# Optimization experiments

Measured on AMD Instinct MI355X. Metric: run time of the kernel, lower is better.

## Reference

```python
import jax, jax.numpy as jnp
import numpy as np

SLOPE = 0.2  # leaky_relu_slope for both LVC block and kernel predictor (passed through)
DILATIONS = (1, 3, 9, 27)
HOP = 256
STRIDE = 8
IN_CH = 32
KSZ = 3  # conv_kernel_size


def conv1d(x, w, b, dilation=1, padding=0):
    # x: (B,C,T), w: (O,I,K) torch layout
    y = jax.lax.conv_general_dilated(
        x, w, window_strides=(1,), padding=[(padding, padding)],
        rhs_dilation=(dilation,), dimension_numbers=('NCH', 'OIH', 'NCH'))
    return y + b[None, :, None]


def conv_transpose1d(x, w, b, stride, padding, output_padding=0):
    # w: torch ConvTranspose1d layout (Cin, Cout, K)
    w_ = jnp.flip(w, -1).transpose(1, 0, 2)  # (Cout, Cin, K)
    K = w.shape[2]
    pad = (K - 1 - padding, K - 1 - padding + output_padding)
    y = jax.lax.conv_general_dilated(
        x, w_, window_strides=(1,), padding=[pad],
        lhs_dilation=(stride,), dimension_numbers=('NCH', 'OIH', 'NCH'))
    return y + b[None, :, None]


def lrelu(x, slope=SLOPE):
    return jnp.where(x >= 0, x, slope * x)


def location_variable_convolution(x, kernel, bias, hop):
    # x: (B,C,T), kernel: (B,C,O,k,L), bias: (B,O,L); T == L*hop; dilation==1 path
    B, C, T = x.shape
    _, _, O, k, L = kernel.shape
    pad = (k - 1) // 2
    xp = jnp.pad(x, ((0, 0), (0, 0), (pad, pad)))
    # gather per-segment sliding windows: (L, hop, k) index into time axis
    idx = (jnp.arange(L)[:, None, None] * hop
           + jnp.arange(hop)[None, :, None]
           + jnp.arange(k)[None, None, :])
    xw = xp[:, :, idx]  # (B, C, L, hop, k)
    o = jnp.einsum('bclsk,bcokl->bols', xw, kernel)  # (B, O, L, hop)
    o = o + bias[:, :, :, None]
    return o.reshape(B, O, L * hop)


def kernel_predictor(spec, kp_in_w, kp_in_b, rb_w1, rb_b1, rb_w2, rb_b2,
                     kern_w, kern_b, bias_w, bias_b):
    B, _, L = spec.shape
    h = conv1d(spec, kp_in_w, kp_in_b, padding=2)  # k=5, pad=2
    for i in range(3):  # num_blocks = 3
        r = h
        h = conv1d(h, rb_w1[i], rb_b1[i], padding=1)
        h = lrelu(h)
        h = conv1d(h, rb_w2[i], rb_b2[i], padding=1)
        h = lrelu(h) + r
    kh = conv1d(h, kern_w, kern_b, padding=1)
    bh = conv1d(h, bias_w, bias_b, padding=1)
    n_layers = len(DILATIONS)
    kernels = kh.reshape(B, n_layers, IN_CH, 2 * IN_CH, KSZ, L)
    biases = bh.reshape(B, n_layers, 2 * IN_CH, L)
    return kernels, biases


def reference(hidden_states, spectrogram, convt_w, convt_b, kp_in_w, kp_in_b,
              rb_w1, rb_b1, rb_w2, rb_b2, kern_w, kern_b, bias_w, bias_b,
              lvc_w, lvc_b):
    h = conv_transpose1d(hidden_states, convt_w, convt_b,
                         stride=STRIDE, padding=STRIDE // 2 + STRIDE % 2,
                         output_padding=STRIDE % 2)
    kernels, biases = kernel_predictor(spectrogram, kp_in_w, kp_in_b,
                                       rb_w1, rb_b1, rb_w2, rb_b2,
                                       kern_w, kern_b, bias_w, bias_b)
    for i, d in enumerate(DILATIONS):
        r = h
        h = lrelu(h)
        h = conv1d(h, lvc_w[i], lvc_b[i], dilation=d, padding=d * (KSZ - 1) // 2)
        h = lrelu(h)
        h = location_variable_convolution(h, kernels[:, i], biases[:, i], HOP)
        h = jax.nn.sigmoid(h[:, :IN_CH, :]) * jnp.tanh(h[:, IN_CH:, :]) + r
    return h


def setup_inputs() -> dict:
    key = jax.random.key(0)
    ks = jax.random.split(key, 12)
    B, COND, L, H = 4, 100, 256, 64
    T = L * HOP  # 65536 output samples
    s = jnp.float32(0.02)
    d = {}
    d['hidden_states'] = jax.random.normal(ks[0], (B, IN_CH, T // STRIDE), jnp.float32)
    d['spectrogram'] = jax.random.normal(ks[1], (B, COND, L), jnp.float32)
    d['convt_w'] = jax.random.normal(ks[2], (IN_CH, IN_CH, 2 * STRIDE), jnp.float32) * s
    d['convt_b'] = jnp.zeros((IN_CH,), jnp.float32)
    d['kp_in_w'] = jax.random.normal(ks[3], (H, COND, 5), jnp.float32) * s
    d['kp_in_b'] = jnp.zeros((H,), jnp.float32)
    d['rb_w1'] = jax.random.normal(ks[4], (3, H, H, 3), jnp.float32) * s
    d['rb_b1'] = jnp.zeros((3, H), jnp.float32)
    d['rb_w2'] = jax.random.normal(ks[5], (3, H, H, 3), jnp.float32) * s
    d['rb_b2'] = jnp.zeros((3, H), jnp.float32)
    KC = IN_CH * 2 * IN_CH * KSZ * len(DILATIONS)  # 24576
    d['kern_w'] = jax.random.normal(ks[6], (KC, H, 3), jnp.float32) * s
    d['kern_b'] = jnp.zeros((KC,), jnp.float32)
    BC = 2 * IN_CH * len(DILATIONS)  # 256
    d['bias_w'] = jax.random.normal(ks[7], (BC, H, 3), jnp.float32) * s
    d['bias_b'] = jnp.zeros((BC,), jnp.float32)
    d['lvc_w'] = jax.random.normal(ks[8], (len(DILATIONS), IN_CH, IN_CH, 3), jnp.float32) * s
    d['lvc_b'] = jnp.zeros((len(DILATIONS), IN_CH), jnp.float32)
    return d
```

## Files before the change

### kernel.cpp

```cpp
#include <hip/hip_runtime.h>
#include <math.h>

#define NB 4
#define T 65536
#define TIN 8192
#define LL 256
#define KCL 6144

__device__ __forceinline__ float lrelu_f(float v) { return v >= 0.f ? v : 0.2f * v; }

union Phase1LDS {
    struct { float xs[32][264]; float wm[64][128]; } cvt;
    struct { float hs[64][56]; float xsp[20][56]; float wt[192][68]; } trk;
};

__global__ void __launch_bounds__(512) phase1(
    const float* __restrict__ x, const float* __restrict__ cw,
    const float* __restrict__ cbias, float* __restrict__ hout,
    const float* __restrict__ spec,
    const float* __restrict__ kp_in_w, const float* __restrict__ kp_in_b,
    const float* __restrict__ rb_w1, const float* __restrict__ rb_b1,
    const float* __restrict__ rb_w2, const float* __restrict__ rb_b2,
    float* __restrict__ kp_h) {
    __shared__ Phase1LDS u;
    const int bid = blockIdx.x;
    const int tid = threadIdx.x;
    const int lane = tid & 63, wv = tid >> 6;

    if (bid < 264) {
        const int bx = bid % 33;
        const int rr = bid / 33;
        const int mtp = rr & 1;
        const int b = rr >> 1;
        const int s0base = bx * 256;
        float (*xs)[264] = u.cvt.xs;
        float (*wm)[128] = u.cvt.wm;

        const float* xb = x + (size_t)b * 32 * TIN;
        for (int idx = tid; idx < 32 * 64; idx += 512) {
            int c = idx >> 6, q = idx & 63;
            int p = s0base + q * 4;
            float4 v = (p + 3 < TIN) ? *(const float4*)(xb + c * TIN + p)
                                     : make_float4(0.f, 0.f, 0.f, 0.f);
            *(float4*)&xs[c][4 + 4 * q] = v;
        }
        if (tid < 32) {
            int p = s0base - 1;
            xs[tid][3] = (p >= 0) ? xb[tid * TIN + p] : 0.f;
        }
        for (int idx = tid; idx < 8192; idx += 512) {
            int i = idx >> 7, mm = idx & 127;
            int oo = mtp * 16 + (mm >> 3), k0 = mm & 7;
            wm[i][mm] = (i < 32) ? cw[i * 512 + oo * 16 + k0]
                                 : cw[(i - 32) * 512 + oo * 16 + k0 + 8];
        }
        __syncthreads();

        float acc[2][8][4];
#pragma unroll
        for (int ol = 0; ol < 2; ++ol) {
            float bo = cbias[mtp * 16 + wv * 2 + ol];
#pragma unroll
            for (int k0 = 0; k0 < 8; ++k0)
#pragma unroll
                for (int si = 0; si < 4; ++si) acc[ol][k0][si] = bo;
        }

        for (int c = 0; c < 32; ++c) {
            float xm1[4], x0[4];
#pragma unroll
            for (int si = 0; si < 4; ++si) {
                xm1[si] = xs[c][lane + si * 64 + 3];
                x0[si]  = xs[c][lane + si * 64 + 4];
            }
            float w0[16], w1[16];
#pragma unroll
            for (int q = 0; q < 4; ++q) {
                *(float4*)&w0[q * 4] = *(const float4*)&wm[c][wv * 16 + q * 4];
                *(float4*)&w1[q * 4] = *(const float4*)&wm[32 + c][wv * 16 + q * 4];
            }
#pragma unroll
            for (int ol = 0; ol < 2; ++ol)
#pragma unroll
                for (int k0 = 0; k0 < 8; ++k0)
#pragma unroll
                    for (int si = 0; si < 4; ++si)
                        acc[ol][k0][si] += x0[si] * w0[ol * 8 + k0] + xm1[si] * w1[ol * 8 + k0];
        }

#pragma unroll
        for (int ol = 0; ol < 2; ++ol) {
            float* ob = hout + ((size_t)b * 32 + mtp * 16 + wv * 2 + ol) * T;
#pragma unroll
            for (int si = 0; si < 4; ++si) {
                int tb = (s0base + lane + si * 64) * 8 - 4;
                if (tb >= 0 && tb < T)
                    *(float4*)(ob + tb) = make_float4(acc[ol][0][si], acc[ol][1][si],
                                                      acc[ol][2][si], acc[ol][3][si]);
                if (tb + 4 >= 0 && tb + 4 < T)
                    *(float4*)(ob + tb + 4) = make_float4(acc[ol][4][si], acc[ol][5][si],
                                                          acc[ol][6][si], acc[ol][7][si]);
            }
        }
        return;
    }

    const int tb = bid - 264;
    const int lq = tb & 7, b = tb >> 3;
    const int j = lane;
    const int oc0 = wv * 8;
    const int l0 = lq * 32;
    const int labs = l0 - 9 + j;
    const bool lvalid = (labs >= 0 && labs < 256);

    float (*hs)[56] = u.trk.hs;
    float (*xsp)[56] = u.trk.xsp;
    float (*wt)[68] = u.trk.wt;

    float pw[24];
    float px[3];

    auto pf_kpin = [&](int cc) {
#pragma unroll
        for (int t = 0; t < 13; ++t) {
            int idx = t * 512 + tid;
            pw[t] = 0.f;
            if (idx < 6400) pw[t] = kp_in_w[(size_t)(idx / 100) * 500 + cc * 100 + (idx % 100)];
        }
    };
    auto wr_kpin = [&]() {
#pragma unroll
        for (int t = 0; t < 13; ++t) {
            int idx = t * 512 + tid;
            if (idx < 6400) wt[idx % 100][idx / 100] = pw[t];
        }
    };
    auto pf_xsp = [&](int cc) {
#pragma unroll
        for (int t = 0; t < 3; ++t) {
            int idx = t * 512 + tid;
            px[t] = 0.f;
            if (idx < 1120) {
                int c = idx / 56, jj = idx - c * 56;
                int l = l0 - 9 + jj;
                if (l >= 0 && l < 256)
                    px[t] = spec[((size_t)b * 100 + cc * 20 + c) * LL + l];
            }
        }
    };
    auto wr_xsp = [&]() {
#pragma unroll
        for (int t = 0; t < 3; ++t) {
            int idx = t * 512 + tid;
            if (idx < 1120) xsp[idx / 56][idx % 56] = px[t];
        }
    };
    auto pf_w192 = [&](const float* src) {
#pragma unroll
        for (int t = 0; t < 24; ++t) pw[t] = src[t * 512 + tid];
    };
    auto wr_w192 = [&]() {
#pragma unroll
        for (int t = 0; t < 24; ++t) {
            int idx = t * 512 + tid;
            wt[idx % 192][idx / 192] = pw[t];
        }
    };
    auto conv64 = [&](int jlo, int jhi, const float* bptr, float* a) {
#pragma unroll
        for (int oi = 0; oi < 8; ++oi) a[oi] = bptr[oc0 + oi];
        if (j >= jlo && j < jhi) {
            for (int c = 0; c < 64; ++c) {
                float x0 = hs[c][j - 1], x1 = hs[c][j], x2 = hs[c][j + 1];
#pragma unroll
                for (int k = 0; k < 3; ++k) {
                    float xk = (k == 0) ? x0 : (k == 1) ? x1 : x2;
                    float w8[8];
                    *(float4*)&w8[0] = *(const float4*)&wt[c * 3 + k][oc0];
                    *(float4*)&w8[4] = *(const float4*)&wt[c * 3 + k][oc0 + 4];
#pragma unroll
                    for (int oi = 0; oi < 8; ++oi) a[oi] += xk * w8[oi];
                }
            }
        }
    };

    pf_kpin(0); pf_xsp(0);
    wr_kpin(); wr_xsp();
    __syncthreads();

    float acc[8];
#pragma unroll
    for (int oi = 0; oi < 8; ++oi) acc[oi] = kp_in_b[oc0 + oi];

    for (int cc = 0; cc < 5; ++cc) {
        if (cc < 4) { pf_kpin(cc + 1); pf_xsp(cc + 1); }
        else        { pf_w192(rb_w1); }
        if (j >= 2 && j < 48) {
            for (int c = 0; c < 20; ++c) {
                float x5[5];
#pragma unroll
                for (int u2 = 0; u2 < 5; ++u2) x5[u2] = xsp[c][j - 2 + u2];
#pragma unroll
                for (int k = 0; k < 5; ++k) {
                    float w8[8];
                    *(float4*)&w8[0] = *(const float4*)&wt[c * 5 + k][oc0];
                    *(float4*)&w8[4] = *(const float4*)&wt[c * 5 + k][oc0 + 4];
#pragma unroll
                    for (int oi = 0; oi < 8; ++oi) acc[oi] += x5[k] * w8[oi];
                }
            }
        }
        if (cc == 4 && j >= 2 && j < 48) {
#pragma unroll
            for (int oi = 0; oi < 8; ++oi) hs[oc0 + oi][j] = lvalid ? acc[oi] : 0.f;
        }
        __syncthreads();
        if (cc < 4) { wr_kpin(); wr_xsp(); }
        else        { wr_w192(); }
        __syncthreads();
    }

    for (int i = 0; i < 3; ++i) {
        const int jlo1 = 3 + 2 * i, jhi1 = 47 - 2 * i;
        const int jlo2 = jlo1 + 1, jhi2 = jhi1 - 1;
        float r[8];
        if (j >= jlo2 && j < jhi2) {
#pragma unroll
            for (int oi = 0; oi < 8; ++oi) r[oi] = hs[oc0 + oi][j];
        }
        pf_w192(rb_w2 + (size_t)i * 12288);
        float a1[8];
        conv64(jlo1, jhi1, rb_b1 + i * 64, a1);
        __syncthreads();
        if (j >= jlo1 && j < jhi1) {
#pragma unroll
            for (int oi = 0; oi < 8; ++oi) hs[oc0 + oi][j] = lvalid ? lrelu_f(a1[oi]) : 0.f;
        }
        wr_w192();
        __syncthreads();
        if (i < 2) pf_w192(rb_w1 + (size_t)(i + 1) * 12288);
        float a2[8];
        conv64(jlo2, jhi2, rb_b2 + i * 64, a2);
        __syncthreads();
        if (j >= jlo2 && j < jhi2) {
#pragma unroll
            for (int oi = 0; oi < 8; ++oi) hs[oc0 + oi][j] = lvalid ? (lrelu_f(a2[oi]) + r[oi]) : 0.f;
        }
        if (i < 2) wr_w192();
        __syncthreads();
    }

    for (int idx = tid; idx < 64 * 32; idx += 512) {
        int c = idx >> 5, jj = idx & 31;
        kp_h[((size_t)b * 64 + c) * LL + l0 + jj] = hs[c][9 + jj];
    }
}

__device__ __forceinline__ void khead_core(
    int bx, int b, int tid,
    const float* __restrict__ kp_h, const float* __restrict__ kw,
    const float* __restrict__ kb, const float* __restrict__ bias_w,
    const float* __restrict__ bias_b, float* __restrict__ kh,
    float* __restrict__ bh, int layer,
    float (*xs)[264], float (*ws)[68]) {
    const bool isbias = (bx >= 96);
    const int lane = tid & 63, wv = tid >> 6;
    int g = 0, ci = 0, kk = 0, ocb0 = 0;
    const float* wsrc;
    size_t wrow0;
    int wstride, nst;
    if (!isbias) {
        g = bx; ci = g / 3; kk = g - ci * 3;
        wsrc = kw + (size_t)layer * KCL * 192;
        wrow0 = (size_t)(ci * 192 + kk) * 192;
        wstride = 576;
        nst = 96 * 64;
    } else {
        ocb0 = (bx - 96) * 32;
        wsrc = bias_w;
        wrow0 = (size_t)ocb0 * 192;
        wstride = 192;
        nst = 96 * 32;
    }
    const int oc8 = wv * 8;
    const int oc4w = wv * 4;

    float acc[8][4];
#pragma unroll
    for (int oi = 0; oi < 8; ++oi) {
        float bv;
        if (isbias) bv = (oi < 4) ? bias_b[ocb0 + oc4w + oi] : 0.f;
        else        bv = kb[layer * KCL + (ci * 64 + oc8 + oi) * 3 + kk];
#pragma unroll
        for (int si = 0; si < 4; ++si) acc[oi][si] = bv;
    }

    for (int half = 0; half < 2; ++half) {
        const int hc0 = half * 32;
        __syncthreads();
        for (int idx = tid; idx < 32 * 64; idx += 512) {
            int c = idx >> 6, q = idx & 63;
            *(float4*)&xs[c][4 + 4 * q] =
                *(const float4*)(kp_h + ((size_t)b * 64 + hc0 + c) * LL + 4 * q);
        }
        if (tid < 32) { xs[tid][3] = 0.f; xs[tid][260] = 0.f; }
        for (int idx = tid; idx < nst; idx += 512) {
            int ocl = idx / 96, jj = idx - ocl * 96;
            ws[jj][ocl] = wsrc[wrow0 + (size_t)ocl * wstride + hc0 * 3 + jj];
        }
        __syncthreads();
        if (!isbias) {
            for (int c = 0; c < 32; ++c) {
#pragma unroll
                for (int t = 0; t < 3; ++t) {
                    float w8[8];
                    *(float4*)&w8[0] = *(const float4*)&ws[c * 3 + t][oc8];
                    *(float4*)&w8[4] = *(const float4*)&ws[c * 3 + t][oc8 + 4];
                    float xv[4];
#pragma unroll
                    for (int si = 0; si < 4; ++si) xv[si] = xs[c][lane + si * 64 + t + 3];
#pragma unroll
                    for (int oi = 0; oi < 8; ++oi)
#pragma unroll
                        for (int si = 0; si < 4; ++si)
                            acc[oi][si] += w8[oi] * xv[si];
                }
            }
        } else {
            for (int c = 0; c < 32; ++c) {
#pragma unroll
                for (int t = 0; t < 3; ++t) {
                    float4 w4 = *(const float4*)&ws[c * 3 + t][oc4w];
                    float xv[4];
#pragma unroll
                    for (int si = 0; si < 4; ++si) xv[si] = xs[c][lane + si * 64 + t + 3];
#pragma unroll
                    for (int si = 0; si < 4; ++si) {
                        acc[0][si] += w4.x * xv[si];
                        acc[1][si] += w4.y * xv[si];
                        acc[2][si] += w4.z * xv[si];
                        acc[3][si] += w4.w * xv[si];
                    }
                }
            }
        }
    }

    if (!isbias) {
#pragma unroll
        for (int si = 0; si < 4; ++si) {
            int l = lane + si * 64;
            float* op = kh + ((size_t)b * LL + l) * KCL + g * 64 + oc8;
            *(float4*)(op)     = make_float4(acc[0][si], acc[1][si], acc[2][si], acc[3][si]);
            *(float4*)(op + 4) = make_float4(acc[4][si], acc[5][si], acc[6][si], acc[7][si]);
        }
    } else {
#pragma unroll
        for (int oi = 0; oi < 4; ++oi) {
            float* op = bh + ((size_t)b * 256 + ocb0 + oc4w + oi) * LL;
#pragma unroll
            for (int si = 0; si < 4; ++si)
                op[lane + si * 64] = acc[oi][si];
        }
    }
}

__global__ void __launch_bounds__(512, 2) kern_head512(
    const float* __restrict__ kp_h, const float* __restrict__ kw,
    const float* __restrict__ kb, const float* __restrict__ bias_w,
    const float* __restrict__ bias_b, float* __restrict__ kh,
    float* __restrict__ bh, int layer) {
    __shared__ float xs[32][264];
    __shared__ float ws[96][68];
    khead_core(blockIdx.x, blockIdx.y, threadIdx.x, kp_h, kw, kb, bias_w, bias_b,
               kh, bh, layer, xs, ws);
}

__device__ __forceinline__ void lf_core(
    int l, int b, int tid,
    const float* __restrict__ kh, const float* __restrict__ bh,
    const float* __restrict__ w, const float* __restrict__ bias,
    const float* __restrict__ hin, float* __restrict__ hout,
    int layer, int dil,
    float (*xh)[316], float* ks, float (*ws)[36]) {
    const int lane = tid & 63, wv = tid >> 6;
    const int t0 = l * 256;

    const float* hb = hin + (size_t)b * 32 * T;
    for (int idx = tid; idx < 32 * 64; idx += 512) {
        int c = idx >> 6, q = idx & 63;
        float4 v = *(const float4*)(hb + (size_t)c * T + t0 + 4 * q);
        *(float4*)&xh[c][32 + 4 * q] = make_float4(lrelu_f(v.x), lrelu_f(v.y),
                                                   lrelu_f(v.z), lrelu_f(v.w));
    }
    for (int idx = tid; idx < 32 * 60; idx += 512) {
        int c = idx / 60, r = idx - c * 60;
        int jj = (r < 32) ? r : (256 + r);
        int t = t0 + jj - 32;
        xh[c][jj] = (t >= 0 && t < T) ? lrelu_f(hb[(size_t)c * T + t]) : 0.f;
    }
    {
        const float4* kp = (const float4*)(kh + ((size_t)b * LL + l) * KCL);
        float4* kd = (float4*)ks;
        for (int idx = tid; idx < KCL / 4; idx += 512) kd[idx] = kp[idx];
    }
    for (int idx = tid; idx < 3072; idx += 512) {
        int oc = idx / 96, ck = idx - oc * 96;
        ws[ck][oc] = w[oc * 96 + ck];
    }
    __syncthreads();

    const int oc4 = wv * 4;
    float yv[5][4];
    {
        float a[5][4];
#pragma unroll
        for (int oi = 0; oi < 4; ++oi) {
            float bv = bias[oc4 + oi];
#pragma unroll
            for (int si = 0; si < 5; ++si) a[si][oi] = bv;
        }
        for (int c = 0; c < 32; ++c) {
#pragma unroll
            for (int k = 0; k < 3; ++k) {
                float4 wq = *(const float4*)&ws[c * 3 + k][oc4];
                float xv[5];
#pragma unroll
                for (int si = 0; si < 5; ++si) {
                    int col = lane + si * 64;
                    int colc = (col < 258) ? col : 257;
                    xv[si] = xh[c][colc + 31 + (k - 1) * dil];
                }
#pragma unroll
                for (int si = 0; si < 5; ++si) {
                    a[si][0] += xv[si] * wq.x;
                    a[si][1] += xv[si] * wq.y;
                    a[si][2] += xv[si] * wq.z;
                    a[si][3] += xv[si] * wq.w;
                }
            }
        }
#pragma unroll
        for (int si = 0; si < 5; ++si) {
            int t = t0 - 1 + lane + si * 64;
            bool tval = (t >= 0 && t < T);
#pragma unroll
            for (int oi = 0; oi < 4; ++oi)
                yv[si][oi] = tval ? lrelu_f(a[si][oi]) : 0.f;
        }
    }
    __syncthreads();

#pragma unroll
    for (int si = 0; si < 5; ++si) {
        int col = lane + si * 64;
        if (col < 258) {
#pragma unroll
            for (int oi = 0; oi < 4; ++oi) xh[oc4 + oi][col + 31] = yv[si][oi];
        }
    }
    __syncthreads();

    float acc_a[4][4], acc_g[4][4];
#pragma unroll
    for (int oi = 0; oi < 4; ++oi) {
        float ba = bh[((size_t)b * 256 + layer * 64 + oc4 + oi) * LL + l];
        float bg = bh[((size_t)b * 256 + layer * 64 + 32 + oc4 + oi) * LL + l];
#pragma unroll
        for (int si = 0; si < 4; ++si) { acc_a[oi][si] = ba; acc_g[oi][si] = bg; }
    }

    for (int c = 0; c < 32; ++c) {
#pragma unroll
        for (int k = 0; k < 3; ++k) {
            const float* kr = ks + (c * 3 + k) * 64;
            float4 wa = *(const float4*)(kr + oc4);
            float4 wg = *(const float4*)(kr + 32 + oc4);
            float xv[4];
#pragma unroll
            for (int si = 0; si < 4; ++si)
                xv[si] = xh[c][lane + si * 64 + k + 31];
#pragma unroll
            for (int si = 0; si < 4; ++si) {
                acc_a[0][si] += wa.x * xv[si];
                acc_a[1][si] += wa.y * xv[si];
                acc_a[2][si] += wa.z * xv[si];
                acc_a[3][si] += wa.w * xv[si];
                acc_g[0][si] += wg.x * xv[si];
                acc_g[1][si] += wg.y * xv[si];
                acc_g[2][si] += wg.z * xv[si];
                acc_g[3][si] += wg.w * xv[si];
            }
        }
    }

#pragma unroll
    for (int oi = 0; oi < 4; ++oi) {
        const float* hip = hin + ((size_t)b * 32 + oc4 + oi) * T + t0;
        float* hop = hout + ((size_t)b * 32 + oc4 + oi) * T + t0;
#pragma unroll
        for (int si = 0; si < 4; ++si) {
            int s = lane + si * 64;
            float a = acc_a[oi][si], g = acc_g[oi][si];
            float sg = 1.f / (1.f + __expf(-a));
            float th = tanhf(g);
            hop[s] = sg * th + hip[s];
        }
    }
}

union FusedLDS {
    struct { float xh[32][316]; float ks[KCL]; float ws[96][36]; } lf;
    struct { float xs[32][264]; float ws[96][68]; } kh;
};

__global__ void __launch_bounds__(512, 2) fused(
    const float* __restrict__ kp_h, const float* __restrict__ kw,
    const float* __restrict__ kb, const float* __restrict__ bias_w,
    const float* __restrict__ bias_b,
    const float* __restrict__ kh_rd, float* __restrict__ kh_wr,
    float* __restrict__ bh,
    const float* __restrict__ lvcw, const float* __restrict__ lvcb,
    const float* __restrict__ hin, float* __restrict__ hout,
    int lf_layer, int dil, int kh_on) {
    __shared__ FusedLDS u;
    const int g = blockIdx.x;
    const int tid = threadIdx.x;
    if (kh_on) {
        const int r = g % 11, q11 = g / 11;
        if (r < 3) {
            const int ukh = q11 * 3 + r;
            const int bx = ukh % 96, b = ukh / 96;
            khead_core(bx, b, tid, kp_h, kw, kb, bias_w, bias_b,
                       kh_wr, bh, lf_layer + 1, u.kh.xs, u.kh.ws);
            return;
        }
        const int ulf = q11 * 8 + (r - 3);
        lf_core(ulf & 255, ulf >> 8, tid, kh_rd, bh, lvcw, lvcb,
                hin, hout, lf_layer, dil, u.lf.xh, u.lf.ks, u.lf.ws);
    } else {
        lf_core(g & 255, g >> 8, tid, kh_rd, bh, lvcw, lvcb,
                hin, hout, lf_layer, dil, u.lf.xh, u.lf.ks, u.lf.ws);
    }
}

extern "C" void kernel_launch(void* const* d_in, const int* in_sizes, int n_in,
                              void* d_out, int out_size, void* d_ws, size_t ws_size,
                              hipStream_t stream) {
    const float* hidden  = (const float*)d_in[0];
    const float* spec    = (const float*)d_in[1];
    const float* convt_w = (const float*)d_in[2];
    const float* convt_b = (const float*)d_in[3];
    const float* kp_in_w = (const float*)d_in[4];
    const float* kp_in_b = (const float*)d_in[5];
    const float* rb_w1   = (const float*)d_in[6];
    const float* rb_b1   = (const float*)d_in[7];
    const float* rb_w2   = (const float*)d_in[8];
    const float* rb_b2   = (const float*)d_in[9];
    const float* kern_w  = (const float*)d_in[10];
    const float* kern_b  = (const float*)d_in[11];
    const float* bias_w  = (const float*)d_in[12];
    const float* bias_b  = (const float*)d_in[13];
    const float* lvc_w   = (const float*)d_in[14];
    const float* lvc_b   = (const float*)d_in[15];

    const size_t NH  = (size_t)NB * 32 * T;
    const size_t NKH = (size_t)NB * LL * KCL;
    const size_t NBH = (size_t)NB * 256 * LL;
    const size_t NKP = (size_t)NB * 64 * LL;
    const size_t need_pp = (NH + 2 * NKH + NBH + NKP) * sizeof(float);
    const bool pp = ws_size >= need_pp;

    float* wsp  = (float*)d_ws;
    float* h_ws = wsp;
    float* kh0  = h_ws + NH;
    float* kh1  = pp ? (kh0 + NKH) : kh0;
    float* bh   = (pp ? kh1 : kh0) + NKH;
    float* kp_h = bh + NBH;

    float* h0 = (float*)d_out;
    float* h1 = h_ws;

    phase1<<<dim3(296), 512, 0, stream>>>(hidden, convt_w, convt_b, h0,
                                          spec, kp_in_w, kp_in_b,
                                          rb_w1, rb_b1, rb_w2, rb_b2, kp_h);

    kern_head512<<<dim3(104, NB), 512, 0, stream>>>(
        kp_h, kern_w, kern_b, bias_w, bias_b, kh0, bh, 0);

    static const int dil[4] = {1, 3, 9, 27};
    float* hin = h0;
    float* hout = h1;
    for (int l = 0; l < 4; ++l) {
        const float* rd = (l & 1) ? kh1 : kh0;
        float* wr = (l & 1) ? kh0 : kh1;
        if (pp && l < 3) {
            fused<<<dim3(1408), 512, 0, stream>>>(
                kp_h, kern_w, kern_b, bias_w, bias_b, rd, wr, bh,
                lvc_w + (size_t)l * 32 * 32 * 3, lvc_b + l * 32,
                hin, hout, l, dil[l], 1);
        } else {
            fused<<<dim3(1024), 512, 0, stream>>>(
                kp_h, kern_w, kern_b, bias_w, bias_b, rd, (float*)rd, bh,
                lvc_w + (size_t)l * 32 * 32 * 3, lvc_b + l * 32,
                hin, hout, l, dil[l], 0);
            if (!pp && l < 3)
                kern_head512<<<dim3(96, NB), 512, 0, stream>>>(
                    kp_h, kern_w, kern_b, bias_w, bias_b, kh0, bh, l + 1);
        }
        float* tmp = hin; hin = hout; hout = tmp;
    }
}
```

Before: 667.5 us.

## Remap residual-block convs to lane-per-channel, six time positions per wave

The residual-block 3-tap convolutions in the kernel predictor are reorganized so each lane owns one output channel and each wave covers six consecutive time positions, replacing the layout where each lane owned a time position and eight output channels. Each lane now reads an 8-wide input window per input channel and reuses it across three taps and six outputs, with one scalar weight per tap. This also keeps all lanes busy instead of masking out the edge positions. The hs row stride is padded to 57 and zero-initialized so the new strided accesses avoid LDS bank conflicts and can safely read past the valid range.

```diff
diff --git a/kernel.cpp b/kernel.cpp
--- a/kernel.cpp
+++ b/kernel.cpp
@@ -11,7 +11,7 @@
 
 union Phase1LDS {
     struct { float xs[32][264]; float wm[64][128]; } cvt;
-    struct { float hs[64][56]; float xsp[20][56]; float wt[192][68]; } trk;
+    struct { float hs[64][57]; float xsp[20][56]; float wt[192][68]; } trk;
 };
 
 __global__ void __launch_bounds__(512) phase1(
@@ -113,12 +113,14 @@
     const int labs = l0 - 9 + j;
     const bool lvalid = (labs >= 0 && labs < 256);
 
-    float (*hs)[56] = u.trk.hs;
+    float (*hs)[57] = u.trk.hs;
     float (*xsp)[56] = u.trk.xsp;
     float (*wt)[68] = u.trk.wt;
 
     float pw[24];
     float px[3];
+
+    for (int idx = tid; idx < 64 * 57; idx += 512) ((float*)hs)[idx] = 0.f;
 
     auto pf_kpin = [&](int cc) {
 #pragma unroll
@@ -166,22 +168,23 @@
             wt[idx % 192][idx / 192] = pw[t];
         }
     };
-    auto conv64 = [&](int jlo, int jhi, const float* bptr, float* a) {
-#pragma unroll
-        for (int oi = 0; oi < 8; ++oi) a[oi] = bptr[oc0 + oi];
-        if (j >= jlo && j < jhi) {
-            for (int c = 0; c < 64; ++c) {
-                float x0 = hs[c][j - 1], x1 = hs[c][j], x2 = hs[c][j + 1];
-#pragma unroll
-                for (int k = 0; k < 3; ++k) {
-                    float xk = (k == 0) ? x0 : (k == 1) ? x1 : x2;
-                    float w8[8];
-                    *(float4*)&w8[0] = *(const float4*)&wt[c * 3 + k][oc0];
-                    *(float4*)&w8[4] = *(const float4*)&wt[c * 3 + k][oc0 + 4];
-#pragma unroll
-                    for (int oi = 0; oi < 8; ++oi) a[oi] += xk * w8[oi];
-                }
-            }
+
+    const int jb = wv * 6;
+    auto conv64n = [&](int jlo, const float* bptr, float* a ) {
+        float bv = bptr[lane];
+#pragma unroll
+        for (int q = 0; q < 6; ++q) a[q] = bv;
+        const int jbase = jlo + jb;
+        for (int c = 0; c < 64; ++c) {
+            float xw[8];
+#pragma unroll
+            for (int q = 0; q < 8; ++q) xw[q] = hs[c][jbase - 1 + q];
+            float w0 = wt[c * 3 + 0][lane];
+            float w1 = wt[c * 3 + 1][lane];
+            float w2 = wt[c * 3 + 2][lane];
+#pragma unroll
+            for (int q = 0; q < 6; ++q)
+                a[q] += xw[q] * w0 + xw[q + 1] * w1 + xw[q + 2] * w2;
         }
     };
 
@@ -224,28 +227,37 @@
     for (int i = 0; i < 3; ++i) {
         const int jlo1 = 3 + 2 * i, jhi1 = 47 - 2 * i;
         const int jlo2 = jlo1 + 1, jhi2 = jhi1 - 1;
-        float r[8];
-        if (j >= jlo2 && j < jhi2) {
-#pragma unroll
-            for (int oi = 0; oi < 8; ++oi) r[oi] = hs[oc0 + oi][j];
-        }
+        const int jbase1 = jlo1 + jb, jbase2 = jlo2 + jb;
+
+        float r6[6];
+#pragma unroll
+        for (int q = 0; q < 6; ++q) r6[q] = hs[lane][jbase2 + q];
+
         pf_w192(rb_w2 + (size_t)i * 12288);
-        float a1[8];
-        conv64(jlo1, jhi1, rb_b1 + i * 64, a1);
-        __syncthreads();
-        if (j >= jlo1 && j < jhi1) {
-#pragma unroll
-            for (int oi = 0; oi < 8; ++oi) hs[oc0 + oi][j] = lvalid ? lrelu_f(a1[oi]) : 0.f;
+        float a1[6];
+        conv64n(jlo1, rb_b1 + i * 64, a1);
+        __syncthreads();
+#pragma unroll
+        for (int q = 0; q < 6; ++q) {
+            int jq = jbase1 + q;
+            if (jq < jhi1) {
+                int la = l0 - 9 + jq;
+                hs[lane][jq] = (la >= 0 && la < 256) ? lrelu_f(a1[q]) : 0.f;
+            }
         }
         wr_w192();
         __syncthreads();
         if (i < 2) pf_w192(rb_w1 + (size_t)(i + 1) * 12288);
-        float a2[8];
-        conv64(jlo2, jhi2, rb_b2 + i * 64, a2);
-        __syncthreads();
-        if (j >= jlo2 && j < jhi2) {
-#pragma unroll
-            for (int oi = 0; oi < 8; ++oi) hs[oc0 + oi][j] = lvalid ? (lrelu_f(a2[oi]) + r[oi]) : 0.f;
+        float a2[6];
+        conv64n(jlo2, rb_b2 + i * 64, a2);
+        __syncthreads();
+#pragma unroll
+        for (int q = 0; q < 6; ++q) {
+            int jq = jbase2 + q;
+            if (jq < jhi2) {
+                int la = l0 - 9 + jq;
+                hs[lane][jq] = (la >= 0 && la < 256) ? (lrelu_f(a2[q]) + r6[q]) : 0.f;
+            }
         }
         if (i < 2) wr_w192();
         __syncthreads();
```

Result: no change. 671.6 us (+0.6%).
